# Kernel tuning notes

Measured on AMD Instinct MI355X. Metric: run time of the kernel, lower is better.

Reference implementation:

```python
import jax, jax.numpy as jnp
import numpy as np

N_NODES = 20000
N_EDGES = 200000
N_GRAPHS = 128
IN_DIM = 256
HID = 512
HEADS = 8
C = HID // HEADS  # 64
LAT = 256
NEG_SLOPE = 0.2
BN_EPS = 1e-5


def setup_inputs() -> dict:
    key = jax.random.key(0)
    ks = jax.random.split(key, 24)
    n = lambda k, s, sc=0.05: jax.random.normal(k, s, jnp.float32) * sc
    return {
        'x': jax.random.normal(ks[0], (N_NODES, IN_DIM), jnp.float32),
        'edge_index': jax.random.randint(ks[1], (2, N_EDGES), 0, N_NODES, jnp.int32),
        'batch': jnp.sort(jax.random.randint(ks[2], (N_NODES,), 0, N_GRAPHS, jnp.int32)),
        'Wl0': n(ks[3], (IN_DIM, HID)), 'bl0': n(ks[4], (HID,)),
        'Wr0': n(ks[5], (IN_DIM, HID)), 'br0': n(ks[6], (HID,)),
        'att0': n(ks[7], (HEADS, C)), 'bias0': n(ks[8], (HID,)),
        'Wl1': n(ks[9], (HID, HID)), 'bl1': n(ks[10], (HID,)),
        'Wr1': n(ks[11], (HID, HID)), 'br1': n(ks[12], (HID,)),
        'att1': n(ks[13], (HEADS, C)), 'bias1': n(ks[14], (HID,)),
        'bn_gamma': jnp.ones((HID,), jnp.float32),
        'bn_beta': jnp.zeros((HID,), jnp.float32),
        'bn_mean': n(ks[15], (HID,)),
        'bn_var': jax.random.uniform(ks[16], (HID,), jnp.float32, 0.5, 1.5),
        'Wfc': n(ks[17], (HID, LAT)), 'bfc': n(ks[18], (LAT,)),
    }


def gatv2_layer(x, src, dst, Wl, bl, Wr, br, att, bias):
    # x: [N, F]; returns [N, HEADS*C]. GATv2: e = a . LeakyReLU(Wl x_src + Wr x_dst)
    xl = (x @ Wl + bl).reshape(-1, HEADS, C)  # source transform [N,H,C]
    xr = (x @ Wr + br).reshape(-1, HEADS, C)  # target transform [N,H,C]
    feat = jax.nn.leaky_relu(xl[src] + xr[dst], NEG_SLOPE)     # [E,H,C]
    logits = jnp.einsum('ehc,hc->eh', feat, att)               # [E,H]
    # segment softmax over incoming edges of each target node
    m = jax.ops.segment_max(logits, dst, num_segments=N_NODES)  # [N,H]
    p = jnp.exp(logits - m[dst])
    denom = jax.ops.segment_sum(p, dst, num_segments=N_NODES)   # [N,H]
    alpha = p / (denom[dst] + 1e-16)                            # [E,H]
    msg = xl[src] * alpha[:, :, None]                           # [E,H,C]
    out = jax.ops.segment_sum(msg, dst, num_segments=N_NODES)   # [N,H,C]
    return out.reshape(-1, HEADS * C) + bias


def reference(x, edge_index, batch, Wl0, bl0, Wr0, br0, att0, bias0,
              Wl1, bl1, Wr1, br1, att1, bias1,
              bn_gamma, bn_beta, bn_mean, bn_var, Wfc, bfc):
    src, dst = edge_index[0], edge_index[1]
    # layer 0 + ELU (dropout is identity in eval mode)
    h = jax.nn.elu(gatv2_layer(x, src, dst, Wl0, bl0, Wr0, br0, att0, bias0))
    # layer 1 + ELU
    h = jax.nn.elu(gatv2_layer(h, src, dst, Wl1, bl1, Wr1, br1, att1, bias1))
    # global add pool over graphs
    g = jax.ops.segment_sum(h, batch, num_segments=N_GRAPHS)  # [G, HID]
    # BatchNorm1d (eval mode: running stats)
    g = (g - bn_mean) * jax.lax.rsqrt(bn_var + BN_EPS) * bn_gamma + bn_beta
    return g @ Wfc + bfc  # [G, LAT]
```

## Files before the change

kernel.cpp:

```cpp
#include <hip/hip_runtime.h>
#include <hip/hip_bf16.h>
#include <cstdint>

#define NN 20000
#define NE 200000
#define NG 128
#define HID 512
#define XLR_W 1024

typedef __attribute__((ext_vector_type(4))) float f32x4;
typedef __attribute__((ext_vector_type(8))) short s16x8;

__device__ __forceinline__ float bf2f(unsigned short u) {
  union { unsigned int i; float f; } v; v.i = ((unsigned int)u) << 16; return v.f;
}
__device__ __forceinline__ unsigned short f2bf(float f) {
  union { float f; unsigned int i; } v; v.f = f;
  unsigned int i = v.i + 0x7FFFu + ((v.i >> 16) & 1u);
  return (unsigned short)(i >> 16);
}
__device__ __forceinline__ float asf(unsigned int u) {
  union { unsigned int i; float f; } v; v.i = u; return v.f;
}

#define GLOAD16(gp, lp)                                                        \
  __builtin_amdgcn_global_load_lds(                                            \
      (const __attribute__((address_space(1))) unsigned int*)(gp),             \
      (__attribute__((address_space(3))) unsigned int*)(lp), 16, 0, 0)

__global__ __launch_bounds__(256) void k_prep(const float* __restrict__ x,
                                              unsigned short* __restrict__ xb,
                                              const float* __restrict__ Wl0, const float* __restrict__ bl0,
                                              const float* __restrict__ Wr0, const float* __restrict__ br0,
                                              unsigned short* __restrict__ wt0, float* __restrict__ bcat0,
                                              const float* __restrict__ Wl1, const float* __restrict__ bl1,
                                              const float* __restrict__ Wr1, const float* __restrict__ br1,
                                              unsigned short* __restrict__ wt1, float* __restrict__ bcat1,
                                              int* __restrict__ deg,
                                              unsigned long long* __restrict__ st) {
  int b = blockIdx.x, t = threadIdx.x;
  if (b < 79) {
    int i = b * 256 + t;
    if (i < NN) deg[i] = 0;
  } else if (b == 79) {
    if (t < 32) st[t] = 0ULL;
  } else if (b < 5080) {
    int i = (b - 80) * 256 + t;
    float4 v = ((const float4*)x)[i];
    ushort4 o;
    o.x = f2bf(v.x); o.y = f2bf(v.y); o.z = f2bf(v.z); o.w = f2bf(v.w);
    ((ushort4*)xb)[i] = o;
  } else if (b < 6104) {
    int id = (b - 5080) * 256 + t;
    int nrow = id >> 8, k = id & 255;
    float v = (nrow < HID) ? Wl0[k * HID + nrow] : Wr0[k * HID + (nrow - HID)];
    wt0[id] = f2bf(v);
    if (id < XLR_W) bcat0[id] = (id < HID) ? bl0[id] : br0[id - HID];
  } else {
    int id = (b - 6104) * 256 + t;
    int nrow = id >> 9, k = id & 511;
    float v = (nrow < HID) ? Wl1[k * HID + nrow] : Wr1[k * HID + (nrow - HID)];
    wt1[id] = f2bf(v);
    if (id < XLR_W) bcat1[id] = (id < HID) ? bl1[id] : br1[id - HID];
  }
}

__global__ __launch_bounds__(1024) void k_scan(const int* __restrict__ deg,
                                               int* __restrict__ offs,
                                               int* __restrict__ woff,
                                               unsigned long long* __restrict__ st,
                                               int n) {
  __shared__ int wsum[16];
  __shared__ int sexcl;
  int t = threadIdx.x;
  int wid = t >> 6, lane = t & 63;
  int i = blockIdx.x * 1024 + t;
  int v = (i < n) ? deg[i] : 0;
  int s = v;
#pragma unroll
  for (int off = 1; off < 64; off <<= 1) {
    int x = __shfl_up(s, off, 64);
    if (lane >= off) s += x;
  }
  if (lane == 63) wsum[wid] = s;
  __syncthreads();
  if (wid == 0) {
    int ws = (lane < 16) ? wsum[lane] : 0;
#pragma unroll
    for (int off = 1; off < 16; off <<= 1) {
      int x = __shfl_up(ws, off, 64);
      if (lane >= off) ws += x;
    }
    if (lane < 16) wsum[lane] = ws;
  }
  __syncthreads();
  int ex = s - v + (wid ? wsum[wid - 1] : 0);
  int bt = wsum[15];
  if (t == 1023) {
    int excl = 0;
    int bid = blockIdx.x;
    if (bid > 0) {
      unsigned long long val;
      do { val = atomicAdd(&st[bid - 1], 0ULL); } while (!(val >> 63));
      excl = (int)(val & 0xFFFFFFFFULL);
    }
    atomicExch(&st[blockIdx.x], (1ULL << 63) | (unsigned long long)(unsigned)(excl + bt));
    sexcl = excl;
    if (bid == (int)gridDim.x - 1) offs[n] = excl + bt;
  }
  __syncthreads();
  int base = sexcl;
  if (i < n) {
    int val = ex + base;
    offs[i] = val;
    woff[i] = val;
  }
}

__global__ void k_scatter(const int* __restrict__ src, const int* __restrict__ dst,
                          int* __restrict__ woff, int* __restrict__ src_s, int E) {
  int i = blockIdx.x * blockDim.x + threadIdx.x;
  if (i < E) {
    int d = dst[i];
    int pos = atomicAdd(&woff[d], 1);
    src_s[pos] = src[i];
  }
}

#define BM 128
#define BN 128
#define PLN 4096

__global__ __launch_bounds__(256) void k_gemm(const unsigned short* __restrict__ A,
                                              const unsigned short* __restrict__ Bt,
                                              const float* __restrict__ bias,
                                              unsigned short* __restrict__ C,
                                              int M, int N, int K, int nby,
                                              const int* __restrict__ hdst,
                                              int* __restrict__ deg,
                                              int gemmBlocks, int histN) {
  __shared__ __align__(16) unsigned short As[2 * PLN];
  __shared__ __align__(16) unsigned short Bs[2 * PLN];
  int L = blockIdx.x;
  if (L >= gemmBlocks) {
    int i = (L - gemmBlocks) * 256 + threadIdx.x;
    if (i < histN) atomicAdd(&deg[hdst[i]], 1);
    return;
  }
  int by = (L & 7) | ((L >> 6) << 3);
  int bx = (L >> 3) & 7;
  if (by >= nby) return;
  int m0 = by * BM, n0 = bx * BN;

  int t = threadIdx.x;
  int wave = t >> 6, lane = t & 63;
  int wm = (wave >> 1) * 64, wn = (wave & 1) * 64;
  int ml = lane & 15, mq = lane >> 4;
  int lr = lane >> 2;
  int qg = (lane & 3) ^ ((lane >> 3) & 3);
  int lq = qg * 8;

  f32x4 acc[4][4];
#pragma unroll
  for (int i = 0; i < 4; i++)
#pragma unroll
    for (int j = 0; j < 4; j++) acc[i][j] = (f32x4)0.0f;

  const unsigned short* gA[4];
  const unsigned short* gB[4];
  unsigned short* lA[4];
  unsigned short* lB[4];
#pragma unroll
  for (int p = 0; p < 2; p++)
#pragma unroll
    for (int h = 0; h < 2; h++) {
      int idx = p * 2 + h;
      int arow = m0 + wave * 32 + h * 16 + lr; if (arow > M - 1) arow = M - 1;
      gA[idx] = A + (size_t)arow * K + p * 32 + lq;
      gB[idx] = Bt + (size_t)(n0 + wave * 32 + h * 16 + lr) * K + p * 32 + lq;
      lA[idx] = &As[p * PLN + (wave * 32 + h * 16) * 32];
      lB[idx] = &Bs[p * PLN + (wave * 32 + h * 16) * 32];
    }

  int qr = (mq ^ ((ml >> 1) & 3)) * 8;

  int T = K >> 6;
  for (int tt = 0; tt < T; tt++) {
#pragma unroll
    for (int idx = 0; idx < 4; idx++) {
      GLOAD16(gA[idx], lA[idx]);
      GLOAD16(gB[idx], lB[idx]);
      gA[idx] += 64; gB[idx] += 64;
    }
    __syncthreads();
#pragma unroll
    for (int kq = 0; kq < 2; kq++) {
      s16x8 af[4], bfr[4];
#pragma unroll
      for (int i = 0; i < 4; i++)
        af[i] = *(const s16x8*)(&As[kq * PLN + (wm + i * 16 + ml) * 32 + qr]);
#pragma unroll
      for (int j = 0; j < 4; j++)
        bfr[j] = *(const s16x8*)(&Bs[kq * PLN + (wn + j * 16 + ml) * 32 + qr]);
#pragma unroll
      for (int i = 0; i < 4; i++)
#pragma unroll
        for (int j = 0; j < 4; j++)
          acc[i][j] = __builtin_amdgcn_mfma_f32_16x16x32_bf16(af[i], bfr[j], acc[i][j], 0, 0, 0);
    }
    __syncthreads();
  }

#pragma unroll
  for (int i = 0; i < 4; i++) {
#pragma unroll
    for (int j = 0; j < 4; j++) {
      int col = n0 + wn + j * 16 + ml;
      float bcol = bias[col];
#pragma unroll
      for (int r = 0; r < 4; r++) {
        int row = m0 + wm + i * 16 + mq * 4 + r;
        if (row < M) C[(size_t)row * N + col] = f2bf(acc[i][j][r] + bcol);
      }
    }
  }
}

__global__ __launch_bounds__(256) void k_attn(const unsigned short* __restrict__ xlr,
                                              const float* __restrict__ att,
                                              const int* __restrict__ offs,
                                              const int* __restrict__ src_s,
                                              const float* __restrict__ bias,
                                              unsigned short* __restrict__ hout) {
  __shared__ float red[4][8][68];
  __shared__ float reds[4][8];
  int n = blockIdx.x;
  int wave = threadIdx.x >> 6, lane = threadIdx.x & 63;
  int h = lane >> 3, k = lane & 7;
  int c = h * 64 + k * 8;
  int s0 = offs[n], s1 = offs[n + 1];

  uint4 uxr = *(const uint4*)(xlr + (size_t)n * XLR_W + HID + c);
  float xr[8];
  xr[0] = asf(uxr.x << 16); xr[1] = asf(uxr.x & 0xFFFF0000u);
  xr[2] = asf(uxr.y << 16); xr[3] = asf(uxr.y & 0xFFFF0000u);
  xr[4] = asf(uxr.z << 16); xr[5] = asf(uxr.z & 0xFFFF0000u);
  xr[6] = asf(uxr.w << 16); xr[7] = asf(uxr.w & 0xFFFF0000u);
  float at[8];
  {
    const float4* ap = (const float4*)(att + c);
    float4 a0 = ap[0], a1 = ap[1];
    at[0] = a0.x; at[1] = a0.y; at[2] = a0.z; at[3] = a0.w;
    at[4] = a1.x; at[5] = a1.y; at[6] = a1.z; at[7] = a1.w;
  }

  float acc[8] = {0.f, 0.f, 0.f, 0.f, 0.f, 0.f, 0.f, 0.f};
  float sum = 0.0f;

  int i = s0 + wave;
  uint4 u_cur = make_uint4(0, 0, 0, 0);
  if (i < s1) {
    int s = src_s[i];
    u_cur = *(const uint4*)(xlr + (size_t)s * XLR_W + c);
  }
  int nx = i + 4;
  for (; i < s1; i += 4) {
    uint4 u = u_cur;
    if (nx < s1) {
      int s = src_s[nx];
      u_cur = *(const uint4*)(xlr + (size_t)s * XLR_W + c);
    }
    nx += 4;

    float xl[8];
    xl[0] = asf(u.x << 16); xl[1] = asf(u.x & 0xFFFF0000u);
    xl[2] = asf(u.y << 16); xl[3] = asf(u.y & 0xFFFF0000u);
    xl[4] = asf(u.z << 16); xl[5] = asf(u.z & 0xFFFF0000u);
    xl[6] = asf(u.w << 16); xl[7] = asf(u.w & 0xFFFF0000u);

    float l = 0.0f;
#pragma unroll
    for (int j = 0; j < 8; j++) {
      float v = xl[j] + xr[j];
      v = fmaf(0.4f, fabsf(v), 0.6f * v);
      l = fmaf(v, at[j], l);
    }
    l += __shfl_xor(l, 1, 64);
    l += __shfl_xor(l, 2, 64);
    l += __shfl_xor(l, 4, 64);

    float p = __expf(l);
    sum += p;
#pragma unroll
    for (int j = 0; j < 8; j++) acc[j] = fmaf(p, xl[j], acc[j]);
  }

#pragma unroll
  for (int j = 0; j < 8; j++) red[wave][h][k * 8 + j] = acc[j];
  if (k == 0) reds[wave][h] = sum;
  __syncthreads();

  int t = threadIdx.x;
  int cc = t * 2;
  int hh = cc >> 6, off = cc & 63;
  float a0 = red[0][hh][off] + red[1][hh][off] + red[2][hh][off] + red[3][hh][off];
  float a1 = red[0][hh][off + 1] + red[1][hh][off + 1] + red[2][hh][off + 1] + red[3][hh][off + 1];
  float sm = reds[0][hh] + reds[1][hh] + reds[2][hh] + reds[3][hh];
  float di = 1.0f / (sm + 1e-16f);
  float o_a = a0 * di + bias[cc];
  float o_b = a1 * di + bias[cc + 1];
  o_a = o_a > 0.0f ? o_a : (__expf(o_a) - 1.0f);
  o_b = o_b > 0.0f ? o_b : (__expf(o_b) - 1.0f);
  unsigned int up = (unsigned int)f2bf(o_a) | ((unsigned int)f2bf(o_b) << 16);
  *(unsigned int*)(hout + (size_t)n * HID + cc) = up;
}

__device__ __forceinline__ int lower_bound(const int* __restrict__ a, int n, int key) {
  int lo = 0, hi = n;
  while (lo < hi) { int mid = (lo + hi) >> 1; if (a[mid] < key) lo = mid + 1; else hi = mid; }
  return lo;
}

__global__ __launch_bounds__(256) void k_poolfc(const unsigned short* __restrict__ h,
                                                const int* __restrict__ batch,
                                                const float* __restrict__ gamma,
                                                const float* __restrict__ beta,
                                                const float* __restrict__ mean,
                                                const float* __restrict__ var,
                                                const float* __restrict__ Wfc,
                                                const float* __restrict__ bfc,
                                                float* __restrict__ out) {
  __shared__ float xsm[512];
  int g = blockIdx.x, t = threadIdx.x;
  int start = lower_bound(batch, NN, g);
  int end = lower_bound(batch, NN, g + 1);
  int c = t * 2;
  float a0 = 0.0f, a1 = 0.0f;
  for (int n = start; n < end; n++) {
    unsigned int u = *(const unsigned int*)(h + (size_t)n * HID + c);
    a0 += asf(u << 16);
    a1 += asf(u & 0xFFFF0000u);
  }
  xsm[c]     = (a0 - mean[c]) * rsqrtf(var[c] + 1e-5f) * gamma[c] + beta[c];
  xsm[c + 1] = (a1 - mean[c + 1]) * rsqrtf(var[c + 1] + 1e-5f) * gamma[c + 1] + beta[c + 1];
  __syncthreads();
  float acc = bfc[t];
#pragma unroll 8
  for (int k = 0; k < 512; k++) acc += xsm[k] * Wfc[k * 256 + t];
  out[g * 256 + t] = acc;
}

extern "C" void kernel_launch(void* const* d_in, const int* in_sizes, int n_in,
                              void* d_out, int out_size, void* d_ws, size_t ws_size,
                              hipStream_t stream) {
  const float* x     = (const float*)d_in[0];
  const int* ei      = (const int*)d_in[1];
  const int* batch   = (const int*)d_in[2];
  const float* Wl0   = (const float*)d_in[3];
  const float* bl0   = (const float*)d_in[4];
  const float* Wr0   = (const float*)d_in[5];
  const float* br0   = (const float*)d_in[6];
  const float* att0  = (const float*)d_in[7];
  const float* bias0 = (const float*)d_in[8];
  const float* Wl1   = (const float*)d_in[9];
  const float* bl1   = (const float*)d_in[10];
  const float* Wr1   = (const float*)d_in[11];
  const float* br1   = (const float*)d_in[12];
  const float* att1  = (const float*)d_in[13];
  const float* bias1 = (const float*)d_in[14];
  const float* gamma = (const float*)d_in[15];
  const float* beta  = (const float*)d_in[16];
  const float* mean  = (const float*)d_in[17];
  const float* var   = (const float*)d_in[18];
  const float* Wfc   = (const float*)d_in[19];
  const float* bfc   = (const float*)d_in[20];

  const int* src = ei;
  const int* dst = ei + NE;

  char* w = (char*)d_ws;
  size_t off = 0;
  auto alloc = [&](size_t bytes) -> void* {
    void* p = w + off;
    off += (bytes + 255) & ~(size_t)255;
    return p;
  };
  int* deg                 = (int*)alloc((size_t)NN * 4);
  int* offs                = (int*)alloc((size_t)(NN + 1) * 4);
  int* woff                = (int*)alloc((size_t)NN * 4);
  int* src_s               = (int*)alloc((size_t)NE * 4);
  unsigned long long* st   = (unsigned long long*)alloc((size_t)32 * 8);
  unsigned short* xb       = (unsigned short*)alloc((size_t)NN * 256 * 2);
  unsigned short* xlr      = (unsigned short*)alloc((size_t)NN * XLR_W * 2);
  unsigned short* hb       = (unsigned short*)alloc((size_t)NN * HID * 2);
  unsigned short* wt0      = (unsigned short*)alloc((size_t)XLR_W * 256 * 2);
  unsigned short* wt1      = (unsigned short*)alloc((size_t)XLR_W * HID * 2);
  float* bcat0             = (float*)alloc((size_t)XLR_W * 4);
  float* bcat1             = (float*)alloc((size_t)XLR_W * 4);

  const int NB   = (NN + 1023) / 1024;
  const int NBY  = (NN + BM - 1) / BM;
  const int GRID = 64 * ((NBY + 7) / 8);
  const int HB   = (NE + 255) / 256;

  k_prep<<<8152, 256, 0, stream>>>(x, xb, Wl0, bl0, Wr0, br0, wt0, bcat0,
                                   Wl1, bl1, Wr1, br1, wt1, bcat1, deg, st);
  k_gemm<<<GRID + HB, 256, 0, stream>>>(xb, wt0, bcat0, xlr, NN, XLR_W, 256, NBY,
                                        dst, deg, GRID, NE);
  k_scan<<<NB, 1024, 0, stream>>>(deg, offs, woff, st, NN);
  k_scatter<<<HB, 256, 0, stream>>>(src, dst, woff, src_s, NE);
  k_attn<<<NN, 256, 0, stream>>>(xlr, att0, offs, src_s, bias0, hb);
  k_gemm<<<GRID, 256, 0, stream>>>(hb, wt1, bcat1, xlr, NN, XLR_W, 512, NBY,
                                   nullptr, nullptr, GRID, 0);
  k_attn<<<NN, 256, 0, stream>>>(xlr, att1, offs, src_s, bias1, hb);
  k_poolfc<<<NG, 256, 0, stream>>>(hb, batch, gamma, beta, mean, var, Wfc, bfc, (float*)d_out);
}
```

Before: 340.8 us.

## Fuse global add-pool into layer-1 attention via atomic accumulation

The second attention kernel now atomically adds its ELU outputs into a per-graph fp32 accumulator instead of writing bf16 node features. A new FC kernel reads those sums, applies batch norm and the final linear layer. The intent is to remove the hidden-feature round trip and the serial per-graph pooling loop. In exchange it issues many contended float atomics and makes the summation order nondeterministic.

```diff
diff --git a/kernel.cpp b/kernel.cpp
--- a/kernel.cpp
+++ b/kernel.cpp
@@ -37,27 +37,31 @@
                                               const float* __restrict__ Wr1, const float* __restrict__ br1,
                                               unsigned short* __restrict__ wt1, float* __restrict__ bcat1,
                                               int* __restrict__ deg,
-                                              unsigned long long* __restrict__ st) {
+                                              unsigned long long* __restrict__ st,
+                                              float* __restrict__ part) {
   int b = blockIdx.x, t = threadIdx.x;
   if (b < 79) {
     int i = b * 256 + t;
     if (i < NN) deg[i] = 0;
   } else if (b == 79) {
     if (t < 32) st[t] = 0ULL;
-  } else if (b < 5080) {
+  } else if (b < 144) {
     int i = (b - 80) * 256 + t;
+    ((float4*)part)[i] = make_float4(0.f, 0.f, 0.f, 0.f);
+  } else if (b < 5144) {
+    int i = (b - 144) * 256 + t;
     float4 v = ((const float4*)x)[i];
     ushort4 o;
     o.x = f2bf(v.x); o.y = f2bf(v.y); o.z = f2bf(v.z); o.w = f2bf(v.w);
     ((ushort4*)xb)[i] = o;
-  } else if (b < 6104) {
-    int id = (b - 5080) * 256 + t;
+  } else if (b < 6168) {
+    int id = (b - 5144) * 256 + t;
     int nrow = id >> 8, k = id & 255;
     float v = (nrow < HID) ? Wl0[k * HID + nrow] : Wr0[k * HID + (nrow - HID)];
     wt0[id] = f2bf(v);
     if (id < XLR_W) bcat0[id] = (id < HID) ? bl0[id] : br0[id - HID];
   } else {
-    int id = (b - 6104) * 256 + t;
+    int id = (b - 6168) * 256 + t;
     int nrow = id >> 9, k = id & 511;
     float v = (nrow < HID) ? Wl1[k * HID + nrow] : Wr1[k * HID + (nrow - HID)];
     wt1[id] = f2bf(v);
@@ -231,7 +235,9 @@
                                               const int* __restrict__ offs,
                                               const int* __restrict__ src_s,
                                               const float* __restrict__ bias,
-                                              unsigned short* __restrict__ hout) {
+                                              unsigned short* __restrict__ hout,
+                                              const int* __restrict__ batch,
+                                              float* __restrict__ part) {
   __shared__ float red[4][8][68];
   __shared__ float reds[4][8];
   int n = blockIdx.x;
@@ -311,38 +317,30 @@
   float o_b = a1 * di + bias[cc + 1];
   o_a = o_a > 0.0f ? o_a : (__expf(o_a) - 1.0f);
   o_b = o_b > 0.0f ? o_b : (__expf(o_b) - 1.0f);
-  unsigned int up = (unsigned int)f2bf(o_a) | ((unsigned int)f2bf(o_b) << 16);
-  *(unsigned int*)(hout + (size_t)n * HID + cc) = up;
-}
-
-__device__ __forceinline__ int lower_bound(const int* __restrict__ a, int n, int key) {
-  int lo = 0, hi = n;
-  while (lo < hi) { int mid = (lo + hi) >> 1; if (a[mid] < key) lo = mid + 1; else hi = mid; }
-  return lo;
-}
-
-__global__ __launch_bounds__(256) void k_poolfc(const unsigned short* __restrict__ h,
-                                                const int* __restrict__ batch,
-                                                const float* __restrict__ gamma,
-                                                const float* __restrict__ beta,
-                                                const float* __restrict__ mean,
-                                                const float* __restrict__ var,
-                                                const float* __restrict__ Wfc,
-                                                const float* __restrict__ bfc,
-                                                float* __restrict__ out) {
+  if (part) {
+    int g = batch[n];
+    atomicAdd(&part[(size_t)g * HID + cc], o_a);
+    atomicAdd(&part[(size_t)g * HID + cc + 1], o_b);
+  } else {
+    unsigned int up = (unsigned int)f2bf(o_a) | ((unsigned int)f2bf(o_b) << 16);
+    *(unsigned int*)(hout + (size_t)n * HID + cc) = up;
+  }
+}
+
+__global__ __launch_bounds__(256) void k_fc(const float* __restrict__ part,
+                                            const float* __restrict__ gamma,
+                                            const float* __restrict__ beta,
+                                            const float* __restrict__ mean,
+                                            const float* __restrict__ var,
+                                            const float* __restrict__ Wfc,
+                                            const float* __restrict__ bfc,
+                                            float* __restrict__ out) {
   __shared__ float xsm[512];
   int g = blockIdx.x, t = threadIdx.x;
-  int start = lower_bound(batch, NN, g);
-  int end = lower_bound(batch, NN, g + 1);
-  int c = t * 2;
-  float a0 = 0.0f, a1 = 0.0f;
-  for (int n = start; n < end; n++) {
-    unsigned int u = *(const unsigned int*)(h + (size_t)n * HID + c);
-    a0 += asf(u << 16);
-    a1 += asf(u & 0xFFFF0000u);
-  }
-  xsm[c]     = (a0 - mean[c]) * rsqrtf(var[c] + 1e-5f) * gamma[c] + beta[c];
-  xsm[c + 1] = (a1 - mean[c + 1]) * rsqrtf(var[c + 1] + 1e-5f) * gamma[c + 1] + beta[c + 1];
+  for (int c = t; c < HID; c += 256) {
+    float s = part[(size_t)g * HID + c];
+    xsm[c] = (s - mean[c]) * rsqrtf(var[c] + 1e-5f) * gamma[c] + beta[c];
+  }
   __syncthreads();
   float acc = bfc[t];
 #pragma unroll 8
@@ -397,21 +395,22 @@
   unsigned short* wt1      = (unsigned short*)alloc((size_t)XLR_W * HID * 2);
   float* bcat0             = (float*)alloc((size_t)XLR_W * 4);
   float* bcat1             = (float*)alloc((size_t)XLR_W * 4);
+  float* part              = (float*)alloc((size_t)NG * HID * 4);
 
   const int NB   = (NN + 1023) / 1024;
   const int NBY  = (NN + BM - 1) / BM;
   const int GRID = 64 * ((NBY + 7) / 8);
   const int HB   = (NE + 255) / 256;
 
-  k_prep<<<8152, 256, 0, stream>>>(x, xb, Wl0, bl0, Wr0, br0, wt0, bcat0,
-                                   Wl1, bl1, Wr1, br1, wt1, bcat1, deg, st);
+  k_prep<<<8216, 256, 0, stream>>>(x, xb, Wl0, bl0, Wr0, br0, wt0, bcat0,
+                                   Wl1, bl1, Wr1, br1, wt1, bcat1, deg, st, part);
   k_gemm<<<GRID + HB, 256, 0, stream>>>(xb, wt0, bcat0, xlr, NN, XLR_W, 256, NBY,
                                         dst, deg, GRID, NE);
   k_scan<<<NB, 1024, 0, stream>>>(deg, offs, woff, st, NN);
   k_scatter<<<HB, 256, 0, stream>>>(src, dst, woff, src_s, NE);
-  k_attn<<<NN, 256, 0, stream>>>(xlr, att0, offs, src_s, bias0, hb);
+  k_attn<<<NN, 256, 0, stream>>>(xlr, att0, offs, src_s, bias0, hb, nullptr, nullptr);
   k_gemm<<<GRID, 256, 0, stream>>>(hb, wt1, bcat1, xlr, NN, XLR_W, 512, NBY,
                                    nullptr, nullptr, GRID, 0);
-  k_attn<<<NN, 256, 0, stream>>>(xlr, att1, offs, src_s, bias1, hb);
-  k_poolfc<<<NG, 256, 0, stream>>>(hb, batch, gamma, beta, mean, var, Wfc, bfc, (float*)d_out);
-}
+  k_attn<<<NN, 256, 0, stream>>>(xlr, att1, offs, src_s, bias1, nullptr, batch, part);
+  k_fc<<<NG, 256, 0, stream>>>(part, gamma, beta, mean, var, Wfc, bfc, (float*)d_out);
+}
```

Result: slower. 364.1 us (+6.8%).
